# Performance work log

Hardware: AMD Instinct MI355X
Metric: run time of the kernel (lower is better)

The kernel has to match this reference:

```python
import jax, jax.numpy as jnp
import numpy as np

K = 16  # neighbors


def _knn_indices(coords, k):
    # coords: (B, 3, N) -> indices (B, N, k) of k nearest points (incl. self)
    sq = jnp.sum(coords * coords, axis=1)                      # (B, N)
    d2 = sq[:, :, None] + sq[:, None, :] - 2.0 * jnp.einsum('bcn,bcm->bnm', coords, coords)
    _, idx = jax.lax.top_k(-d2, k)                             # smallest distances
    return idx


def _gather(points, idx):
    # points: (B, C, N), idx: (B, N, k) -> (B, C, N, k)
    return jax.vmap(lambda p, i: p[:, i])(points, idx)


def setup_inputs() -> dict:
    key = jax.random.key(0)
    ks = jax.random.split(key, 8)
    B, N, C_IN, C_OUT = 4, 8192, 64, 64
    s = 0.05
    return {
        'features': jax.random.normal(ks[0], (B, C_IN, N), dtype=jnp.float32),
        'coords': jax.random.normal(ks[1], (B, 3, N), dtype=jnp.float32),
        'w_lin': jax.random.normal(ks[2], (3 * C_OUT, C_IN), dtype=jnp.float32) * s,
        'w_theta1': jax.random.normal(ks[3], (C_OUT, 3), dtype=jnp.float32) * s,
        'w_theta2': jax.random.normal(ks[4], (C_OUT, C_OUT), dtype=jnp.float32) * s,
        'w_gamma1': jax.random.normal(ks[5], (C_OUT, C_OUT), dtype=jnp.float32) * s,
        'w_gamma2': jax.random.normal(ks[6], (C_OUT, C_OUT), dtype=jnp.float32) * s,
    }


def reference(features, coords, w_lin, w_theta1, w_theta2, w_gamma1, w_gamma2):
    # KNN (int indices, non-differentiable)
    idx = _knn_indices(coords, K)                              # (B, N, k)

    knn_coords = _gather(coords, idx)                          # (B, 3, N, k)
    rel = coords[:, :, :, None] - knn_coords                   # localize * -1
    delta = jnp.einsum('oc,bcnk->bonk', w_theta1, rel)
    delta = jax.nn.relu(jnp.einsum('oc,bcnk->bonk', w_theta2, delta))  # (B, Co, N, k)

    # input linear -> phi, psi, alpha
    feat3 = jnp.einsum('oc,bcn->bon', w_lin, features)         # (B, 3*Co, N)
    phi, psi, alpha = jnp.split(feat3, 3, axis=1)

    psi_g = _gather(psi, idx)                                  # (B, Co, N, k)
    inputs_gamma = phi[:, :, :, None] - psi_g + delta          # localize*-1 + delta
    g = jnp.einsum('oc,bcnk->bonk', w_gamma1, inputs_gamma)
    g = jax.nn.relu(jnp.einsum('oc,bcnk->bonk', w_gamma2, g))
    rho = jax.nn.softmax(g, axis=-1)                           # softmax over k

    alpha_g = _gather(alpha, idx) + delta                      # (B, Co, N, k)
    return jnp.sum(rho * alpha_g, axis=-1)                     # (B, Co, N)
```

## Files before the change

kernel.cpp:

```cpp
#include <hip/hip_runtime.h>
#include <cstdint>


#define NPT 8192
typedef unsigned long long u64;
typedef unsigned int u32;
typedef unsigned short u16;
typedef __attribute__((ext_vector_type(8))) short bf8_t;
typedef __attribute__((ext_vector_type(4))) float f32x4;

__device__ __forceinline__ u16 f2bf(float x) {
  return (u16)((__float_as_uint(x) + 0x8000u) >> 16);
}
__device__ __forceinline__ u32 pkbf(float lo, float hi) {
  return (u32)f2bf(lo) | ((u32)f2bf(hi) << 16);
}
__device__ __forceinline__ float bf2f(u16 v) {
  return __uint_as_float((u32)v << 16);
}
__device__ __forceinline__ u32 med3u(u32 a, u32 b, u32 c) {
  u32 d;
  asm("v_med3_u32 %0, %1, %2, %3" : "=v"(d) : "v"(a), "v"(b), "v"(c));
  return d;
}
__device__ __forceinline__ u32 umin2(u32 a, u32 b) { return a < b ? a : b; }
__device__ __forceinline__ u32 umax2(u32 a, u32 b) { return a > b ? a : b; }
__device__ __forceinline__ float rfl_f(float x) {
  return __uint_as_float((u32)__builtin_amdgcn_readfirstlane((int)__float_as_uint(x)));
}
__device__ __forceinline__ u32 wave_min_u32(u32 v) {
  u32 t;
  t = (u32)__builtin_amdgcn_update_dpp((int)v, (int)v, 0x111, 0xF, 0xF, false); v = umin2(v, t);
  t = (u32)__builtin_amdgcn_update_dpp((int)v, (int)v, 0x112, 0xF, 0xF, false); v = umin2(v, t);
  t = (u32)__builtin_amdgcn_update_dpp((int)v, (int)v, 0x114, 0xF, 0xF, false); v = umin2(v, t);
  t = (u32)__builtin_amdgcn_update_dpp((int)v, (int)v, 0x118, 0xF, 0xF, false); v = umin2(v, t);
  t = (u32)__builtin_amdgcn_update_dpp((int)v, (int)v, 0x142, 0xF, 0xF, false); v = umin2(v, t);
  t = (u32)__builtin_amdgcn_update_dpp((int)v, (int)v, 0x143, 0xF, 0xF, false); v = umin2(v, t);
  return (u32)__builtin_amdgcn_readlane((int)v, 63);
}
__device__ __forceinline__ u32 wave_max_u32(u32 v) {
  u32 t;
  t = (u32)__builtin_amdgcn_update_dpp((int)v, (int)v, 0x111, 0xF, 0xF, false); v = umax2(v, t);
  t = (u32)__builtin_amdgcn_update_dpp((int)v, (int)v, 0x112, 0xF, 0xF, false); v = umax2(v, t);
  t = (u32)__builtin_amdgcn_update_dpp((int)v, (int)v, 0x114, 0xF, 0xF, false); v = umax2(v, t);
  t = (u32)__builtin_amdgcn_update_dpp((int)v, (int)v, 0x118, 0xF, 0xF, false); v = umax2(v, t);
  t = (u32)__builtin_amdgcn_update_dpp((int)v, (int)v, 0x142, 0xF, 0xF, false); v = umax2(v, t);
  t = (u32)__builtin_amdgcn_update_dpp((int)v, (int)v, 0x143, 0xF, 0xF, false); v = umax2(v, t);
  return (u32)__builtin_amdgcn_readlane((int)v, 63);
}
__device__ __forceinline__ void ins8(u32* a, u32 key) {
  a[7] = med3u(key, a[6], a[7]);
  a[6] = med3u(key, a[5], a[6]);
  a[5] = med3u(key, a[4], a[5]);
  a[4] = med3u(key, a[3], a[4]);
  a[3] = med3u(key, a[2], a[3]);
  a[2] = med3u(key, a[1], a[2]);
  a[1] = med3u(key, a[0], a[1]);
  a[0] = umin2(a[0], key);
}

__global__ __launch_bounds__(256) void fold1_k(
    const float* __restrict__ wg1, const float* __restrict__ wg2,
    const float* __restrict__ wt1, const float* __restrict__ wt2,
    float* __restrict__ G, float* __restrict__ Mrow, float* __restrict__ McT) {
  int t = blockIdx.x * 256 + threadIdx.x;
  if (t < 4096) {
    int o = t >> 6, c = t & 63;
    float acc = 0.f;
    for (int cp = 0; cp < 64; ++cp) acc = fmaf(wg2[o * 64 + cp], wg1[cp * 64 + c], acc);
    G[o * 64 + c] = acc;
  } else if (t < 4096 + 192) {
    int i = t - 4096;
    int o = i / 3, j = i - o * 3;
    float acc = 0.f;
    for (int c = 0; c < 64; ++c) acc = fmaf(wt2[o * 64 + c], wt1[c * 3 + j], acc);
    Mrow[o * 3 + j] = acc;
    McT[j * 64 + o] = acc;
  }
}

__global__ __launch_bounds__(256) void fold2_k(
    const float* __restrict__ G, const float* __restrict__ wl,
    u16* __restrict__ GF, u16* __restrict__ WF) {
  int t = blockIdx.x * 256 + threadIdx.x;
  if (t < 12288) {
    int o = t >> 6, c = t & 63;
    float acc = 0.f;
    if (o < 64) {
      for (int cp = 0; cp < 64; ++cp) acc = fmaf(G[o * 64 + cp], wl[cp * 64 + c], acc);
    } else if (o < 128) {
      for (int cp = 0; cp < 64; ++cp) acc = fmaf(G[(o - 64) * 64 + cp], wl[(64 + cp) * 64 + c], acc);
    } else {
      acc = wl[o * 64 + c];
    }
    int ot = o >> 4, m = o & 15;
    int kh = c >> 5, q = (c >> 3) & 3, j = c & 7;
    WF[(((ot * 2 + kh) * 64) + (q * 16 + m)) * 8 + j] = f2bf(acc);
  } else {
    int i = t - 12288;
    int o = i >> 6, c = i & 63;
    int ot = o >> 4, m = o & 15;
    int kh = c >> 5, q = (c >> 3) & 3, j = c & 7;
    GF[(((ot * 2 + kh) * 64) + (q * 16 + m)) * 8 + j] = f2bf(G[o * 64 + c]);
  }
}

__global__ __launch_bounds__(256) void pack_k(const float* __restrict__ coords,
                                              float4* __restrict__ pack) {
  int g = blockIdx.x * 256 + threadIdx.x;
  int b = g >> 13, n = g & (NPT - 1);
  const float* c = coords + (size_t)b * 3 * NPT;
  float x = c[n], y = c[NPT + n], z = c[2 * NPT + n];
  float sq = __fadd_rn(__fadd_rn(__fmul_rn(x, x), __fmul_rn(y, y)), __fmul_rn(z, z));
  pack[g] = make_float4(x, y, z, sq);
}

#define NB 1024
#define XMIN -5.0f
#define BW 0.009765625f
#define INVBW 102.4f
#define NQ 32768

__global__ __launch_bounds__(1024) void zero_k(u32* __restrict__ cnt) {
  cnt[blockIdx.x * 1024 + threadIdx.x] = 0;
}

__global__ __launch_bounds__(256) void cnt_k(const float4* __restrict__ pack,
                                             u32* __restrict__ cnt) {
  int g = blockIdx.x * 256 + threadIdx.x;
  int b = g >> 13;
  float x = pack[g].x;
  int bi = (int)floorf((x - XMIN) * INVBW);
  bi = bi < 0 ? 0 : (bi > NB - 1 ? NB - 1 : bi);
  atomicAdd(&cnt[b * NB + bi], 1u);
}

__global__ __launch_bounds__(1024) void scan_k(const u32* __restrict__ cnt,
                                               u32* __restrict__ cursor) {
  __shared__ u32 S[NB];
  int b = blockIdx.x, t = threadIdx.x;
  u32 own = cnt[b * NB + t];
  S[t] = own;
  __syncthreads();
  for (int off = 1; off < NB; off <<= 1) {
    u32 v = (t >= off) ? S[t - off] : 0u;
    __syncthreads();
    S[t] += v;
    __syncthreads();
  }
  cursor[b * NB + t] = S[t] - own;
}

__global__ __launch_bounds__(256) void scat_k(const float4* __restrict__ pack,
                                              u32* __restrict__ cursor,
                                              float4* __restrict__ spack,
                                              int* __restrict__ sidx,
                                              float* __restrict__ xedge) {
  int g = blockIdx.x * 256 + threadIdx.x;
  int b = g >> 13, n = g & (NPT - 1);
  float4 p = pack[g];
  int bi = (int)floorf((p.x - XMIN) * INVBW);
  bi = bi < 0 ? 0 : (bi > NB - 1 ? NB - 1 : bi);
  u32 pos = atomicAdd(&cursor[b * NB + bi], 1u);
  size_t o = (size_t)b * NPT + pos;
  spack[o] = p;
  sidx[o] = n;
  xedge[o] = fmaf((float)bi, BW, XMIN);
}

#define QW 4
__global__ __launch_bounds__(256) void knn_k(const float4* __restrict__ spack,
                                             const int* __restrict__ sidx,
                                             const float* __restrict__ xedge,
                                             u32* __restrict__ part24) {
  int tid = threadIdx.x;
  int wid = tid >> 6, lane = tid & 63;
  int q0 = blockIdx.x * (4 * QW) + wid * QW;
  int b = q0 >> 13, c0 = q0 & (NPT - 1);
  const float4* sp = spack + (size_t)b * NPT;
  const int* si = sidx + (size_t)b * NPT;
  const float* xe = xedge + (size_t)b * NPT;
  float qx[QW], qy[QW], qz[QW], qs[QW];
#pragma unroll
  for (int j = 0; j < QW; ++j) {
    float4 qv = sp[c0 + j];
    qx[j] = rfl_f(qv.x); qy[j] = rfl_f(qv.y);
    qz[j] = rfl_f(qv.z); qs[j] = rfl_f(qv.w);
  }
  float qxmax = fmaxf(fmaxf(qx[0], qx[1]), fmaxf(qx[2], qx[3]));
  float qxmin = fminf(fminf(qx[0], qx[1]), fminf(qx[2], qx[3]));
  u32 arr[QW][8];
#pragma unroll
  for (int j = 0; j < QW; ++j)
#pragma unroll
    for (int s = 0; s < 8; ++s) arr[j][s] = 0xFFFFFFFFu;
  int R = c0, L = c0;
  bool ra = true, la = (c0 > 0);
#pragma unroll 1
  while (ra || la) {
    if (ra) {
      int cand = R + lane;
      bool ok = cand < NPT;
      int cc = ok ? cand : NPT - 1;
      float4 p = sp[cc];
      u32 ki = (u32)si[cc];
      u32 kbad = ok ? 0u : 0xFFFFFFFFu;
#pragma unroll
      for (int j = 0; j < QW; ++j) {
        float dot = fmaf(qz[j], p.z, fmaf(qy[j], p.y, qx[j] * p.x));
        float d2 = fmaxf(fmaf(-2.f, dot, qs[j] + p.w), 0.f);
        u32 key = ((__float_as_uint(d2) & 0xFFFFE000u) | ki) | kbad;
        ins8(arr[j], key);
      }
      R += 64;
      if (R >= NPT) ra = false;
    }
    if (la) {
      int base = L - 64;
      int cand = base + lane;
      bool ok = cand >= 0;
      int cc = ok ? cand : 0;
      float4 p = sp[cc];
      u32 ki = (u32)si[cc];
      u32 kbad = ok ? 0u : 0xFFFFFFFFu;
#pragma unroll
      for (int j = 0; j < QW; ++j) {
        float dot = fmaf(qz[j], p.z, fmaf(qy[j], p.y, qx[j] * p.x));
        float d2 = fmaxf(fmaf(-2.f, dot, qs[j] + p.w), 0.f);
        u32 key = ((__float_as_uint(d2) & 0xFFFFE000u) | ki) | kbad;
        ins8(arr[j], key);
      }
      L = base;
      if (L <= 0) la = false;
    }
    u32 mx = umax2(umax2(arr[0][0], arr[1][0]), umax2(arr[2][0], arr[3][0]));
    u32 tau = wave_max_u32(mx);
    if (tau < 0xFF000000u) {
      float tf = __uint_as_float((tau & 0xFFFFE000u) + 0x20000u);
      if (ra) {
        float dxr = (xe[R] - 1e-3f) - qxmax;
        if (dxr > 0.f && dxr * dxr > tf) ra = false;
      }
      if (la) {
        float dxl = qxmin - (xe[L - 1] + (BW + 1e-3f));
        if (dxl > 0.f && dxl * dxl > tf) la = false;
      }
    }
  }
#pragma unroll
  for (int j = 0; j < QW; ++j) {
    u32 mg = 0xFFFFFFFFu;
#pragma unroll 1
    for (int r = 0; r < 24; ++r) {
      u32 m = wave_min_u32(arr[j][0]);
      if (lane == r) mg = m;
      if (arr[j][0] == m) {
        arr[j][0] = arr[j][1]; arr[j][1] = arr[j][2];
        arr[j][2] = arr[j][3]; arr[j][3] = arr[j][4];
        arr[j][4] = arr[j][5]; arr[j][5] = arr[j][6];
        arr[j][6] = arr[j][7]; arr[j][7] = 0xFFFFFFFFu;
      }
    }
    if (lane < 24) part24[((size_t)b * NPT + c0 + j) * 24 + lane] = mg;
  }
}

__global__ __launch_bounds__(64) void refine_k(const float4* __restrict__ pack,
                                               const float4* __restrict__ spack,
                                               const int* __restrict__ sidx,
                                               const u32* __restrict__ part24,
                                               int* __restrict__ idxk) {
  int gs = blockIdx.x * 64 + threadIdx.x;
  int b = gs >> 13;
  const float4* pk = pack + (size_t)b * NPT;
  int qid = sidx[gs];
  float4 q = spack[gs];
  float qx = q.x, qy = q.y, qz = q.z, qs = q.w;
  float bd[16];
  int bi[16];
#pragma unroll
  for (int j = 0; j < 16; ++j) { bd[j] = 1e30f; bi[j] = 0x7FFFFFFF; }
#pragma unroll 4
  for (int j = 0; j < 24; ++j) {
    int m = (int)(part24[(size_t)gs * 24 + j] & 0x1FFFu);
    float4 pm = pk[m];
    float dot = __fadd_rn(__fadd_rn(__fmul_rn(qx, pm.x), __fmul_rn(qy, pm.y)),
                          __fmul_rn(qz, pm.z));
    float kd = __fsub_rn(__fadd_rn(qs, pm.w), __fmul_rn(2.0f, dot));
    int ki = m;
    if (kd < bd[15] || (kd == bd[15] && ki < bi[15])) {
#pragma unroll
      for (int qq = 0; qq < 16; ++qq) {
        bool cs = (kd < bd[qq]) || (kd == bd[qq] && ki < bi[qq]);
        float td = bd[qq];
        int ti = bi[qq];
        bd[qq] = cs ? kd : td;
        bi[qq] = cs ? ki : ti;
        kd = cs ? td : kd;
        ki = cs ? ti : ki;
      }
    }
  }
#pragma unroll
  for (int j = 0; j < 16; ++j) idxk[(size_t)(((size_t)b * NPT + qid)) * 16 + j] = bi[j];
}

__global__ __launch_bounds__(256) void feat_k(const float* __restrict__ features,
                                              const u16* __restrict__ WF,
                                              float* __restrict__ featA,
                                              u16* __restrict__ featB) {
  int tid = threadIdx.x;
  int w = tid >> 6, l = tid & 63;
  int quad = l >> 4, col = l & 15;
  int P = blockIdx.x * 64 + w * 16 + col;
  int b = P >> 13, n = P & (NPT - 1);
  const float* fb = features + (size_t)b * 64 * NPT + n;
  const bf8_t* wfr = (const bf8_t*)WF;
  bf8_t Bf[2];
#pragma unroll
  for (int kh = 0; kh < 2; ++kh) {
    union { u32 wv[4]; bf8_t v; } ub;
#pragma unroll
    for (int j2 = 0; j2 < 4; ++j2) {
      float lo = fb[(size_t)(kh * 32 + quad * 8 + j2 * 2) * NPT];
      float hi = fb[(size_t)(kh * 32 + quad * 8 + j2 * 2 + 1) * NPT];
      ub.wv[j2] = pkbf(lo, hi);
    }
    Bf[kh] = ub.v;
  }
#pragma unroll
  for (int ot = 0; ot < 12; ++ot) {
    bf8_t A0 = wfr[(ot * 2 + 0) * 64 + l];
    bf8_t A1 = wfr[(ot * 2 + 1) * 64 + l];
    f32x4 acc = {0.f, 0.f, 0.f, 0.f};
    acc = __builtin_amdgcn_mfma_f32_16x16x32_bf16(A0, Bf[0], acc, 0, 0, 0);
    acc = __builtin_amdgcn_mfma_f32_16x16x32_bf16(A1, Bf[1], acc, 0, 0, 0);
    int gr = ot * 16 + quad * 4;
    if (ot < 4) {
      *(float4*)(featA + (size_t)P * 64 + gr) = make_float4(acc[0], acc[1], acc[2], acc[3]);
    } else {
      uint2 wv2 = make_uint2(pkbf(acc[0], acc[1]), pkbf(acc[2], acc[3]));
      *(uint2*)(featB + (size_t)P * 128 + (gr - 64)) = wv2;
    }
  }
}

#define SROW 68
__global__ __launch_bounds__(64) void attn_k(
    const float4* __restrict__ pack, const int* __restrict__ idxk,
    const float* __restrict__ featA, const u16* __restrict__ featB,
    const u16* __restrict__ GF, const float* __restrict__ Mrow,
    const float* __restrict__ McT, float* __restrict__ out) {
  __shared__ u16 S16[64 * SROW];
  int l = threadIdx.x;
  int quad = l >> 4, col = l & 15;
  int Pb = blockIdx.x * 4;
  int b = Pb >> 13;
  int nb0 = Pb & (NPT - 1);
  const float4* pkb = pack + (size_t)b * NPT;
  int idxv = idxk[(size_t)Pb * 16 + l];
  int mve[4];
#pragma unroll
  for (int t = 0; t < 4; ++t) mve[t] = __shfl(idxv, t * 16 + col);
  float relx[4], rely[4], relz[4];
#pragma unroll
  for (int t = 0; t < 4; ++t) {
    float4 own = pkb[nb0 + t];
    float4 nbr = pkb[mve[t]];
    relx[t] = own.x - nbr.x; rely[t] = own.y - nbr.y; relz[t] = own.z - nbr.z;
  }
  bf8_t Bf[4][2];
#pragma unroll
  for (int kh = 0; kh < 2; ++kh) {
    const float* mr = Mrow + (kh * 32 + quad * 8) * 3;
    float m_[24];
#pragma unroll
    for (int i6 = 0; i6 < 6; ++i6) {
      float4 v = *(const float4*)(mr + i6 * 4);
      m_[i6 * 4] = v.x; m_[i6 * 4 + 1] = v.y; m_[i6 * 4 + 2] = v.z; m_[i6 * 4 + 3] = v.w;
    }
#pragma unroll
    for (int t = 0; t < 4; ++t) {
      float u_[8];
#pragma unroll
      for (int j = 0; j < 8; ++j)
        u_[j] = fmaxf(fmaf(m_[j * 3 + 2], relz[t],
                           fmaf(m_[j * 3 + 1], rely[t], m_[j * 3] * relx[t])), 0.f);
      union { u32 w[4]; bf8_t v; } ub;
#pragma unroll
      for (int j2 = 0; j2 < 4; ++j2) ub.w[j2] = pkbf(u_[j2 * 2], u_[j2 * 2 + 1]);
      Bf[t][kh] = ub.v;
    }
  }
  const bf8_t* gfr = (const bf8_t*)GF;
#pragma unroll
  for (int ot = 0; ot < 4; ++ot) {
    bf8_t A0 = gfr[(ot * 2 + 0) * 64 + l];
    bf8_t A1 = gfr[(ot * 2 + 1) * 64 + l];
#pragma unroll
    for (int pt = 0; pt < 4; ++pt) {
      f32x4 acc = {0.f, 0.f, 0.f, 0.f};
      acc = __builtin_amdgcn_mfma_f32_16x16x32_bf16(A0, Bf[pt][0], acc, 0, 0, 0);
      acc = __builtin_amdgcn_mfma_f32_16x16x32_bf16(A1, Bf[pt][1], acc, 0, 0, 0);
      const float* phn = featA + (size_t)(Pb + pt) * 64 + ot * 16 + quad * 4;
      float4 ph = *(const float4*)phn;
      uint2 psw = *(const uint2*)(featB + ((size_t)b * NPT + mve[pt]) * 128 + ot * 16 + quad * 4);
      float g0 = fmaxf(acc[0] + ph.x - bf2f((u16)(psw.x & 0xFFFF)), 0.f);
      float g1 = fmaxf(acc[1] + ph.y - bf2f((u16)(psw.x >> 16)), 0.f);
      float g2 = fmaxf(acc[2] + ph.z - bf2f((u16)(psw.y & 0xFFFF)), 0.f);
      float g3 = fmaxf(acc[3] + ph.w - bf2f((u16)(psw.y >> 16)), 0.f);
      uint2 wv = make_uint2(pkbf(g0, g1), pkbf(g2, g3));
      *(uint2*)&S16[(pt * 16 + col) * SROW + ot * 16 + quad * 4] = wv;
    }
  }
  __syncthreads();
  float mc0 = McT[l], mc1 = McT[64 + l], mc2 = McT[128 + l];
  float accv[4];
#pragma unroll 1
  for (int pj = 0; pj < 4; ++pj) {
    float4 ownq = pkb[nb0 + pj];
    float gvv[16];
    float mx = -1e30f;
#pragma unroll
    for (int r = 0; r < 16; ++r) {
      gvv[r] = bf2f(S16[(pj * 16 + r) * SROW + l]);
      mx = fmaxf(mx, gvv[r]);
    }
    float s = 0.f;
#pragma unroll
    for (int r = 0; r < 16; ++r) {
      float e = __expf(gvv[r] - mx);
      gvv[r] = e;
      s += e;
    }
    float inv = 1.0f / s;
    float acc = 0.f;
#pragma unroll
    for (int r = 0; r < 16; ++r) {
      int si = __builtin_amdgcn_readlane(idxv, pj * 16 + r);
      float dl = fmaxf(fmaf(mc2, ownq.z - pkb[si].z,
                            fmaf(mc1, ownq.y - pkb[si].y, mc0 * (ownq.x - pkb[si].x))), 0.f);
      float al = bf2f(featB[((size_t)b * NPT + si) * 128 + 64 + l]);
      acc = fmaf(gvv[r] * inv, al + dl, acc);
    }
    accv[pj] = acc;
  }
  *(float4*)(out + ((size_t)b * 64 + l) * NPT + nb0) =
      make_float4(accv[0], accv[1], accv[2], accv[3]);
}

extern "C" void kernel_launch(void* const* d_in, const int* in_sizes, int n_in,
                              void* d_out, int out_size, void* d_ws, size_t ws_size,
                              hipStream_t stream) {
  const float* features = (const float*)d_in[0];
  const float* coords = (const float*)d_in[1];
  const float* w_lin = (const float*)d_in[2];
  const float* w_t1 = (const float*)d_in[3];
  const float* w_t2 = (const float*)d_in[4];
  const float* w_g1 = (const float*)d_in[5];
  const float* w_g2 = (const float*)d_in[6];
  float* out = (float*)d_out;
  char* ws = (char*)d_ws;
  float4* pack = (float4*)ws;
  float* G = (float*)(ws + 524288);
  float* Mrow = (float*)(ws + 540672);
  float* McT = (float*)(ws + 541440);
  int* idxk = (int*)(ws + 591360);
  float* featA = (float*)(ws + 2688512);
  u16* featB = (u16*)(ws + 11077120);
  u32* part24 = (u32*)(ws + 2688512);
  float4* spack = (float4*)(ws + 11077120);
  int* sidx = (int*)(ws + 11601408);
  float* xedge = (float*)(ws + 11732480);
  u32* cnt = (u32*)(ws + 11863552);
  u32* cursor = (u32*)(ws + 11879936);
  u16* GF = (u16*)(ws + 19465728);
  u16* WF = (u16*)(ws + 19473920);

  fold1_k<<<17, 256, 0, stream>>>(w_g1, w_g2, w_t1, w_t2, G, Mrow, McT);
  fold2_k<<<64, 256, 0, stream>>>(G, w_lin, GF, WF);
  pack_k<<<128, 256, 0, stream>>>(coords, pack);
  zero_k<<<4, 1024, 0, stream>>>(cnt);
  cnt_k<<<128, 256, 0, stream>>>(pack, cnt);
  scan_k<<<4, 1024, 0, stream>>>(cnt, cursor);
  scat_k<<<128, 256, 0, stream>>>(pack, cursor, spack, sidx, xedge);
  knn_k<<<2048, 256, 0, stream>>>(spack, sidx, xedge, part24);
  refine_k<<<512, 64, 0, stream>>>(pack, spack, sidx, part24, idxk);
  feat_k<<<512, 256, 0, stream>>>(features, WF, featA, featB);
  attn_k<<<8192, 64, 0, stream>>>(pack, idxk, featA, featB, GF, Mrow, McT, out);
}
```

Measured before the change: 310.1 us.

## Tighten KNN pruning bound, use sorted-slot keys, interleave query-wave order

```diff
diff --git a/kernel.cpp b/kernel.cpp
--- a/kernel.cpp
+++ b/kernel.cpp
@@ -36,16 +36,6 @@
   t = (u32)__builtin_amdgcn_update_dpp((int)v, (int)v, 0x118, 0xF, 0xF, false); v = umin2(v, t);
   t = (u32)__builtin_amdgcn_update_dpp((int)v, (int)v, 0x142, 0xF, 0xF, false); v = umin2(v, t);
   t = (u32)__builtin_amdgcn_update_dpp((int)v, (int)v, 0x143, 0xF, 0xF, false); v = umin2(v, t);
-  return (u32)__builtin_amdgcn_readlane((int)v, 63);
-}
-__device__ __forceinline__ u32 wave_max_u32(u32 v) {
-  u32 t;
-  t = (u32)__builtin_amdgcn_update_dpp((int)v, (int)v, 0x111, 0xF, 0xF, false); v = umax2(v, t);
-  t = (u32)__builtin_amdgcn_update_dpp((int)v, (int)v, 0x112, 0xF, 0xF, false); v = umax2(v, t);
-  t = (u32)__builtin_amdgcn_update_dpp((int)v, (int)v, 0x114, 0xF, 0xF, false); v = umax2(v, t);
-  t = (u32)__builtin_amdgcn_update_dpp((int)v, (int)v, 0x118, 0xF, 0xF, false); v = umax2(v, t);
-  t = (u32)__builtin_amdgcn_update_dpp((int)v, (int)v, 0x142, 0xF, 0xF, false); v = umax2(v, t);
-  t = (u32)__builtin_amdgcn_update_dpp((int)v, (int)v, 0x143, 0xF, 0xF, false); v = umax2(v, t);
   return (u32)__builtin_amdgcn_readlane((int)v, 63);
 }
 __device__ __forceinline__ void ins8(u32* a, u32 key) {
@@ -170,15 +160,16 @@
 
 #define QW 4
 __global__ __launch_bounds__(256) void knn_k(const float4* __restrict__ spack,
-                                             const int* __restrict__ sidx,
                                              const float* __restrict__ xedge,
                                              u32* __restrict__ part24) {
   int tid = threadIdx.x;
   int wid = tid >> 6, lane = tid & 63;
-  int q0 = blockIdx.x * (4 * QW) + wid * QW;
-  int b = q0 >> 13, c0 = q0 & (NPT - 1);
+  int gw = blockIdx.x * 4 + wid;
+  int b = gw >> 11;
+  int gb = gw & 2047;
+  int gbs = (gb & 31) * 64 + (gb >> 5);
+  int c0 = gbs * QW;
   const float4* sp = spack + (size_t)b * NPT;
-  const int* si = sidx + (size_t)b * NPT;
   const float* xe = xedge + (size_t)b * NPT;
   float qx[QW], qy[QW], qz[QW], qs[QW];
 #pragma unroll
@@ -203,13 +194,12 @@
       bool ok = cand < NPT;
       int cc = ok ? cand : NPT - 1;
       float4 p = sp[cc];
-      u32 ki = (u32)si[cc];
       u32 kbad = ok ? 0u : 0xFFFFFFFFu;
 #pragma unroll
       for (int j = 0; j < QW; ++j) {
         float dot = fmaf(qz[j], p.z, fmaf(qy[j], p.y, qx[j] * p.x));
         float d2 = fmaxf(fmaf(-2.f, dot, qs[j] + p.w), 0.f);
-        u32 key = ((__float_as_uint(d2) & 0xFFFFE000u) | ki) | kbad;
+        u32 key = ((__float_as_uint(d2) & 0xFFFFE000u) | (u32)cc) | kbad;
         ins8(arr[j], key);
       }
       R += 64;
@@ -221,22 +211,22 @@
       bool ok = cand >= 0;
       int cc = ok ? cand : 0;
       float4 p = sp[cc];
-      u32 ki = (u32)si[cc];
       u32 kbad = ok ? 0u : 0xFFFFFFFFu;
 #pragma unroll
       for (int j = 0; j < QW; ++j) {
         float dot = fmaf(qz[j], p.z, fmaf(qy[j], p.y, qx[j] * p.x));
         float d2 = fmaxf(fmaf(-2.f, dot, qs[j] + p.w), 0.f);
-        u32 key = ((__float_as_uint(d2) & 0xFFFFE000u) | ki) | kbad;
+        u32 key = ((__float_as_uint(d2) & 0xFFFFE000u) | (u32)cc) | kbad;
         ins8(arr[j], key);
       }
       L = base;
       if (L <= 0) la = false;
     }
-    u32 mx = umax2(umax2(arr[0][0], arr[1][0]), umax2(arr[2][0], arr[3][0]));
-    u32 tau = wave_max_u32(mx);
-    if (tau < 0xFF000000u) {
-      float tf = __uint_as_float((tau & 0xFFFFE000u) + 0x20000u);
+    u32 pm = umax2(umax2(arr[0][7], arr[1][7]), umax2(arr[2][7], arr[3][7]));
+    u32 sw = (u32)__builtin_amdgcn_update_dpp((int)pm, (int)pm, 0xB1, 0xF, 0xF, false);
+    u32 B = wave_min_u32(umax2(pm, sw));
+    if (B < 0xFF000000u) {
+      float tf = __uint_as_float((B & 0xFFFFE000u) + 0x20000u);
       if (ra) {
         float dxr = (xe[R] - 1e-3f) - qxmax;
         if (dxr > 0.f && dxr * dxr > tf) ra = false;
@@ -265,14 +255,14 @@
   }
 }
 
-__global__ __launch_bounds__(64) void refine_k(const float4* __restrict__ pack,
-                                               const float4* __restrict__ spack,
+__global__ __launch_bounds__(64) void refine_k(const float4* __restrict__ spack,
                                                const int* __restrict__ sidx,
                                                const u32* __restrict__ part24,
                                                int* __restrict__ idxk) {
   int gs = blockIdx.x * 64 + threadIdx.x;
   int b = gs >> 13;
-  const float4* pk = pack + (size_t)b * NPT;
+  const float4* sp = spack + (size_t)b * NPT;
+  const int* si = sidx + (size_t)b * NPT;
   int qid = sidx[gs];
   float4 q = spack[gs];
   float qx = q.x, qy = q.y, qz = q.z, qs = q.w;
@@ -282,12 +272,12 @@
   for (int j = 0; j < 16; ++j) { bd[j] = 1e30f; bi[j] = 0x7FFFFFFF; }
 #pragma unroll 4
   for (int j = 0; j < 24; ++j) {
-    int m = (int)(part24[(size_t)gs * 24 + j] & 0x1FFFu);
-    float4 pm = pk[m];
+    int ms = (int)(part24[(size_t)gs * 24 + j] & 0x1FFFu);
+    float4 pm = sp[ms];
+    int ki = si[ms];
     float dot = __fadd_rn(__fadd_rn(__fmul_rn(qx, pm.x), __fmul_rn(qy, pm.y)),
                           __fmul_rn(qz, pm.z));
     float kd = __fsub_rn(__fadd_rn(qs, pm.w), __fmul_rn(2.0f, dot));
-    int ki = m;
     if (kd < bd[15] || (kd == bd[15] && ki < bi[15])) {
 #pragma unroll
       for (int qq = 0; qq < 16; ++qq) {
@@ -484,8 +474,8 @@
   cnt_k<<<128, 256, 0, stream>>>(pack, cnt);
   scan_k<<<4, 1024, 0, stream>>>(cnt, cursor);
   scat_k<<<128, 256, 0, stream>>>(pack, cursor, spack, sidx, xedge);
-  knn_k<<<2048, 256, 0, stream>>>(spack, sidx, xedge, part24);
-  refine_k<<<512, 64, 0, stream>>>(pack, spack, sidx, part24, idxk);
+  knn_k<<<2048, 256, 0, stream>>>(spack, xedge, part24);
+  refine_k<<<512, 64, 0, stream>>>(spack, sidx, part24, idxk);
   feat_k<<<512, 256, 0, stream>>>(features, WF, featA, featB);
   attn_k<<<8192, 64, 0, stream>>>(pack, idxk, featA, featB, GF, Mrow, McT, out);
 }
```

After: 315.8 us. About the same (+1.9%).
